# Optimization experiments

Measured on AMD Instinct MI355X. Metric: run time of the kernel, lower is better.

The kernel has to match this reference:

```python
import jax, jax.numpy as jnp
import numpy as np

B, D, L, H, P, IMG = 32, 768, 12, 12, 16, 224
N = (IMG // P) ** 2  # 196 patches
DH = D // H
FF = 4 * D
EPS = 1e-5


def _ln(x, w, b):
    m = jnp.mean(x, axis=-1, keepdims=True)
    v = jnp.mean((x - m) ** 2, axis=-1, keepdims=True)
    return (x - m) * jax.lax.rsqrt(v + EPS) * w + b


def setup_inputs() -> dict:
    key = jax.random.key(0)
    ks = jax.random.split(key, 12)
    s = 0.02
    return {
        "x": jax.random.normal(ks[0], (B, 3, IMG, IMG), jnp.float32),
        "patch_w": jax.random.normal(ks[1], (D, 3, P, P), jnp.float32) * s,
        "patch_b": jnp.zeros((D,), jnp.float32),
        "pos_embed": jax.random.normal(ks[2], (1, N, D), jnp.float32) * s,
        "ln1_w": jnp.ones((L, D), jnp.float32),
        "ln1_b": jnp.zeros((L, D), jnp.float32),
        "qkv_w": jax.random.normal(ks[3], (L, 3 * D, D), jnp.float32) * s,
        "qkv_b": jnp.zeros((L, 3 * D), jnp.float32),
        "proj_w": jax.random.normal(ks[4], (L, D, D), jnp.float32) * s,
        "proj_b": jnp.zeros((L, D), jnp.float32),
        "ln2_w": jnp.ones((L, D), jnp.float32),
        "ln2_b": jnp.zeros((L, D), jnp.float32),
        "fc1_w": jax.random.normal(ks[5], (L, FF, D), jnp.float32) * s,
        "fc1_b": jnp.zeros((L, FF), jnp.float32),
        "fc2_w": jax.random.normal(ks[6], (L, D, FF), jnp.float32) * s,
        "fc2_b": jnp.zeros((L, D), jnp.float32),
        "lnf_w": jnp.ones((D,), jnp.float32),
        "lnf_b": jnp.zeros((D,), jnp.float32),
    }


def reference(x, patch_w, patch_b, pos_embed, ln1_w, ln1_b, qkv_w, qkv_b,
              proj_w, proj_b, ln2_w, ln2_b, fc1_w, fc1_b, fc2_w, fc2_b,
              lnf_w, lnf_b):
    # Patch embed: strided conv, NCHW / OIHW
    h = jax.lax.conv_general_dilated(
        x, patch_w, window_strides=(P, P), padding="VALID",
        dimension_numbers=("NCHW", "OIHW", "NCHW")) + patch_b[None, :, None, None]
    b = h.shape[0]
    h = h.reshape(b, D, -1).transpose(0, 2, 1)  # (B, N, D)
    h = h + pos_embed  # broadcast over batch

    scale = DH ** (-0.5)
    for i in range(L):
        # --- attention (indices=None path: plain masked-free softmax) ---
        y = _ln(h, ln1_w[i], ln1_b[i])
        qkv = y @ qkv_w[i].T + qkv_b[i]                      # (B, N, 3D)
        qkv = qkv.reshape(b, -1, 3, H, DH).transpose(2, 0, 3, 1, 4)
        q, k, v = qkv[0], qkv[1], qkv[2]                     # (B, H, N, DH)
        attn = jax.nn.softmax(jnp.einsum("bhnd,bhmd->bhnm", q, k) * scale, axis=-1)
        o = jnp.einsum("bhnm,bhmd->bhnd", attn, v)
        o = o.transpose(0, 2, 1, 3).reshape(b, -1, D)
        h = h + (o @ proj_w[i].T + proj_b[i])
        # --- MLP ---
        y = _ln(h, ln2_w[i], ln2_b[i])
        y = jax.nn.gelu(y @ fc1_w[i].T + fc1_b[i], approximate=False)
        h = h + (y @ fc2_w[i].T + fc2_b[i])

    return _ln(h, lnf_w, lnf_b)
```

## Files before the change

### kernel.cpp

```cpp
#include <hip/hip_runtime.h>
#include <hip/hip_bf16.h>
#include <math.h>

#define BB    32
#define DD    768
#define LL    12
#define HH    12
#define NN    196
#define DHH   64
#define FFF   3072
#define MM    (BB * NN)
#define BHH   (BB * HH)

typedef float  floatx4 __attribute__((ext_vector_type(4)));
typedef __bf16 bf16x8  __attribute__((ext_vector_type(8)));

#define DEV __device__ __forceinline__

DEV unsigned short bf16u(float v) {
  __hip_bfloat16 h = __float2bfloat16(v);
  return __builtin_bit_cast(unsigned short, h);
}

DEV floatx4 mfma_bf16(bf16x8 a, bf16x8 b, floatx4 c) {
  return __builtin_amdgcn_mfma_f32_16x16x32_bf16(a, b, c, 0, 0, 0);
}

DEV void gl2lds16(const void* g, void* l) {
  __builtin_amdgcn_global_load_lds(
      (const __attribute__((address_space(1))) void*)g,
      (__attribute__((address_space(3))) void*)l, 16, 0, 0);
}

DEV float gelu_f(float v) {
  float ax = fabsf(v) * 0.70710678118654752f;
  float t = 1.0f / (1.0f + 0.3275911f * ax);
  float poly = t * (0.254829592f +
              t * (-0.284496736f +
              t * (1.421413741f +
              t * (-1.453152027f +
              t * 1.061405429f))));
  float er = 1.0f - poly * __expf(-ax * ax);
  er = (v < 0.0f) ? -er : er;
  return 0.5f * v * (1.0f + er);
}

DEV int xcd_swz(int orig, int nwg) {
  int q = nwg >> 3, r = nwg & 7;
  int xcd = orig & 7, pos = orig >> 3;
  int base = (xcd < r) ? xcd * (q + 1) : r * (q + 1) + (xcd - r) * q;
  return base + pos;
}

__global__ __launch_bounds__(256) void cvt4_k(const float4* __restrict__ in,
                                              ushort4* __restrict__ out, int n4) {
  int i = blockIdx.x * 256 + threadIdx.x;
  if (i < n4) {
    float4 v = in[i];
    ushort4 o;
    o.x = bf16u(v.x); o.y = bf16u(v.y); o.z = bf16u(v.z); o.w = bf16u(v.w);
    out[i] = o;
  }
}

__global__ __launch_bounds__(256) void im2col_k(const float* __restrict__ x,
                                                unsigned short* __restrict__ A) {
  int idx = blockIdx.x * 256 + threadIdx.x;
  int col = idx % DD;
  int token = idx / DD;
  int b = token / NN, p = token % NN;
  int pr = p / 14, pc = p % 14;
  int c = col >> 8, rm = col & 255, i = rm >> 4, j = rm & 15;
  float v = x[(((size_t)b * 3 + c) * 224 + pr * 16 + i) * 224 + pc * 16 + j];
  A[idx] = bf16u(v);
}

__global__ __launch_bounds__(256) void ln_k(const float* __restrict__ x,
                                            const float* __restrict__ w,
                                            const float* __restrict__ bb,
                                            unsigned short* __restrict__ outp) {
  const int token = blockIdx.x, tid = threadIdx.x;
  const float* xr = x + (size_t)token * DD;
  float v0 = xr[tid], v1 = xr[tid + 256], v2 = xr[tid + 512];
  float s = v0 + v1 + v2;
  float ss = v0 * v0 + v1 * v1 + v2 * v2;
#pragma unroll
  for (int off = 32; off; off >>= 1) {
    s += __shfl_down(s, off);
    ss += __shfl_down(ss, off);
  }
  __shared__ float rs[4], rq[4];
  if ((tid & 63) == 0) { rs[tid >> 6] = s; rq[tid >> 6] = ss; }
  __syncthreads();
  float tot = rs[0] + rs[1] + rs[2] + rs[3];
  float tq  = rq[0] + rq[1] + rq[2] + rq[3];
  const float mean = tot * (1.0f / 768.0f);
  const float var  = tq * (1.0f / 768.0f) - mean * mean;
  const float rstd = rsqrtf(var + 1e-5f);
#pragma unroll
  for (int t = 0; t < 3; t++) {
    int col = tid + t * 256;
    float xv = (t == 0) ? v0 : (t == 1 ? v1 : v2);
    float yv = (xv - mean) * rstd * w[col] + bb[col];
    outp[(size_t)token * DD + col] = bf16u(yv);
  }
}

template <int FINAL>
__global__ __launch_bounds__(256) void ln_fuse_k(float* __restrict__ h,
    const float* __restrict__ p0, const float* __restrict__ p1,
    const float* __restrict__ w, const float* __restrict__ bb,
    void* __restrict__ outp) {
  const int token = blockIdx.x, tid = threadIdx.x;
  const size_t base = (size_t)token * DD;
  float v[3];
#pragma unroll
  for (int t = 0; t < 3; t++) {
    const int col = tid + t * 256;
    v[t] = h[base + col] + p0[base + col] + p1[base + col];
    if (!FINAL) h[base + col] = v[t];
  }
  float s = v[0] + v[1] + v[2];
  float ss = v[0] * v[0] + v[1] * v[1] + v[2] * v[2];
#pragma unroll
  for (int off = 32; off; off >>= 1) {
    s += __shfl_down(s, off);
    ss += __shfl_down(ss, off);
  }
  __shared__ float rs[4], rq[4];
  if ((tid & 63) == 0) { rs[tid >> 6] = s; rq[tid >> 6] = ss; }
  __syncthreads();
  float tot = rs[0] + rs[1] + rs[2] + rs[3];
  float tq  = rq[0] + rq[1] + rq[2] + rq[3];
  const float mean = tot * (1.0f / 768.0f);
  const float var  = tq * (1.0f / 768.0f) - mean * mean;
  const float rstd = rsqrtf(var + 1e-5f);
#pragma unroll
  for (int t = 0; t < 3; t++) {
    const int col = tid + t * 256;
    float yv = (v[t] - mean) * rstd * w[col] + bb[col];
    if (FINAL) ((float*)outp)[base + col] = yv;
    else       ((unsigned short*)outp)[base + col] = bf16u(yv);
  }
}


template <int MODE>
__global__ __launch_bounds__(256, 4) void gemm_bt(
    const unsigned short* __restrict__ A, const unsigned short* __restrict__ W,
    const float* __restrict__ bias, void* __restrict__ outp, int K, int Nn) {
  __shared__ unsigned short smem[16384];
  unsigned short* As0 = smem;
  unsigned short* Bs0 = smem + 8192;
  const int tid = threadIdx.x;
  const int wave = tid >> 6, lane = tid & 63;
  const int nwg = gridDim.x * gridDim.y;
  const int wg = xcd_swz(blockIdx.x + gridDim.x * blockIdx.y, nwg);
  const int tm = (wg / gridDim.x) * 128, tn = (wg % gridDim.x) * 128;
  const int wm = (wave >> 1) * 64, wn = (wave & 1) * 64;
  const int lr = lane & 15, kq = lane >> 4;
  const int sw = (lr >> 1) & 3;
  const int koff = (kq ^ sw) * 8;
  const int c0 = tid, c1 = tid + 256;
  const int r0 = c0 >> 2, r1 = c1 >> 2;
  const int kc0 = ((c0 & 3) ^ ((r0 >> 1) & 3)) * 8;
  const int kc1 = ((c1 & 3) ^ ((r1 >> 1) & 3)) * 8;
  const size_t ga0 = (size_t)(tm + r0) * K + kc0;
  const size_t ga1 = (size_t)(tm + r1) * K + kc1;
  const size_t gb0 = (size_t)(tn + r0) * K + kc0;
  const size_t gb1 = (size_t)(tn + r1) * K + kc1;
  floatx4 acc[4][4] = {};
  auto stage = [&](int buf, int k0) {
    gl2lds16(A + ga0 + k0, As0 + buf * 4096 + c0 * 8);
    gl2lds16(A + ga1 + k0, As0 + buf * 4096 + c1 * 8);
    gl2lds16(W + gb0 + k0, Bs0 + buf * 4096 + c0 * 8);
    gl2lds16(W + gb1 + k0, Bs0 + buf * 4096 + c1 * 8);
  };
  const int nk = K >> 5;
  stage(0, 0);
  for (int it = 0; it < nk; it++) {
    const int cur = it & 1;
    __syncthreads();
    if (it + 1 < nk) stage(cur ^ 1, (it + 1) << 5);
    bf16x8 af[4], bq[4];
#pragma unroll
    for (int mi = 0; mi < 4; mi++)
      af[mi] = *(const bf16x8*)&As0[cur * 4096 + (wm + mi * 16 + lr) * 32 + koff];
#pragma unroll
    for (int ni = 0; ni < 4; ni++)
      bq[ni] = *(const bf16x8*)&Bs0[cur * 4096 + (wn + ni * 16 + lr) * 32 + koff];
#pragma unroll
    for (int mi = 0; mi < 4; mi++)
#pragma unroll
      for (int ni = 0; ni < 4; ni++)
        acc[mi][ni] = mfma_bf16(af[mi], bq[ni], acc[mi][ni]);
  }
  __syncthreads();
#pragma unroll
  for (int ni = 0; ni < 4; ni++) {
    const int lcol = wn + ni * 16 + lr;
    const float bv = bias[tn + lcol];
#pragma unroll
    for (int mi = 0; mi < 4; mi++) {
#pragma unroll
      for (int r = 0; r < 4; r++) {
        const int lrow = wm + mi * 16 + (lane >> 4) * 4 + r;
        float v = acc[mi][ni][r] + bv;
        if (MODE == 3) v = gelu_f(v);
        smem[lrow * 128 + lcol] = bf16u(v);
      }
    }
  }
  __syncthreads();
  const int tr = tid >> 4;
  const int tc = (tid & 15) * 8;
#pragma unroll
  for (int p = 0; p < 8; p++) {
    const int lrow = p * 16 + tr;
    uint4 d = *(const uint4*)&smem[lrow * 128 + tc];
    *(uint4*)&((unsigned short*)outp)[(size_t)(tm + lrow) * Nn + tn + tc] = d;
  }
}

__global__ __launch_bounds__(256, 4) void gemm_sk(
    const unsigned short* __restrict__ A, const unsigned short* __restrict__ W,
    const float* __restrict__ bias, float* __restrict__ p0,
    float* __restrict__ p1, int K, int Nn) {
  __shared__ unsigned short As[2][128 * 32];
  __shared__ unsigned short Bs[2][128 * 32];
  const int tid = threadIdx.x;
  const int wave = tid >> 6, lane = tid & 63;
  const int nwg = gridDim.x * gridDim.y;
  const int wg = xcd_swz(blockIdx.x + gridDim.x * blockIdx.y, nwg);
  const int tm = (wg / gridDim.x) * 128, tn = (wg % gridDim.x) * 128;
  const int kz = blockIdx.z;
  const int kper = K >> 1;
  const int kbase = kz * kper;
  const int wm = (wave >> 1) * 64, wn = (wave & 1) * 64;
  const int lr = lane & 15, kq = lane >> 4;
  const int sw = (lr >> 1) & 3;
  const int koff = (kq ^ sw) * 8;
  const int c0 = tid, c1 = tid + 256;
  const int r0 = c0 >> 2, r1 = c1 >> 2;
  const int kc0 = ((c0 & 3) ^ ((r0 >> 1) & 3)) * 8;
  const int kc1 = ((c1 & 3) ^ ((r1 >> 1) & 3)) * 8;
  const size_t ga0 = (size_t)(tm + r0) * K + kc0 + kbase;
  const size_t ga1 = (size_t)(tm + r1) * K + kc1 + kbase;
  const size_t gb0 = (size_t)(tn + r0) * K + kc0 + kbase;
  const size_t gb1 = (size_t)(tn + r1) * K + kc1 + kbase;
  floatx4 acc[4][4] = {};
  auto stage = [&](int buf, int k0) {
    gl2lds16(A + ga0 + k0, &As[buf][c0 * 8]);
    gl2lds16(A + ga1 + k0, &As[buf][c1 * 8]);
    gl2lds16(W + gb0 + k0, &Bs[buf][c0 * 8]);
    gl2lds16(W + gb1 + k0, &Bs[buf][c1 * 8]);
  };
  const int nk = kper >> 5;
  stage(0, 0);
  for (int it = 0; it < nk; it++) {
    const int cur = it & 1;
    __syncthreads();
    if (it + 1 < nk) stage(cur ^ 1, (it + 1) << 5);
    bf16x8 af[4], bq[4];
#pragma unroll
    for (int mi = 0; mi < 4; mi++)
      af[mi] = *(const bf16x8*)&As[cur][(wm + mi * 16 + lr) * 32 + koff];
#pragma unroll
    for (int ni = 0; ni < 4; ni++)
      bq[ni] = *(const bf16x8*)&Bs[cur][(wn + ni * 16 + lr) * 32 + koff];
#pragma unroll
    for (int mi = 0; mi < 4; mi++)
#pragma unroll
      for (int ni = 0; ni < 4; ni++)
        acc[mi][ni] = mfma_bf16(af[mi], bq[ni], acc[mi][ni]);
  }
  float* __restrict__ po = kz ? p1 : p0;
  const int rbase = tm + wm + (lane >> 4) * 4;
  const int cbase = tn + wn + lr;
#pragma unroll
  for (int ni = 0; ni < 4; ni++) {
    const int col = cbase + ni * 16;
    const float bv = kz ? 0.0f : bias[col];
#pragma unroll
    for (int mi = 0; mi < 4; mi++) {
#pragma unroll
      for (int r = 0; r < 4; r++) {
        const int row = rbase + mi * 16 + r;
        po[(size_t)row * Nn + col] = acc[mi][ni][r] + bv;
      }
    }
  }
}

template <int MODE>
__global__ __launch_bounds__(256, 4) void gemm64_bt(
    const unsigned short* __restrict__ A, const unsigned short* __restrict__ W,
    const float* __restrict__ bias, const float* __restrict__ aux,
    float* __restrict__ outp, int K, int Nn) {
  __shared__ unsigned short As[2][64 * 32];
  __shared__ unsigned short Bs[2][128 * 32];
  const int tid = threadIdx.x;
  const int wave = tid >> 6, lane = tid & 63;
  const int tm = blockIdx.y * 64, tn = blockIdx.x * 128;
  const int wm = (wave >> 1) * 32, wn = (wave & 1) * 64;
  const int lr = lane & 15, kq = lane >> 4;
  const int sw = (lr >> 1) & 3;
  const int koff = (kq ^ sw) * 8;
  const int ra = tid >> 2;
  const int kca = ((tid & 3) ^ ((ra >> 1) & 3)) * 8;
  const int c0 = tid, c1 = tid + 256;
  const int r0 = c0 >> 2, r1 = c1 >> 2;
  const int kc0 = ((c0 & 3) ^ ((r0 >> 1) & 3)) * 8;
  const int kc1 = ((c1 & 3) ^ ((r1 >> 1) & 3)) * 8;
  const size_t ga  = (size_t)(tm + ra) * K + kca;
  const size_t gb0 = (size_t)(tn + r0) * K + kc0;
  const size_t gb1 = (size_t)(tn + r1) * K + kc1;
  floatx4 acc[2][4] = {};
  auto stage = [&](int buf, int k0) {
    gl2lds16(A + ga + k0, &As[buf][tid * 8]);
    gl2lds16(W + gb0 + k0, &Bs[buf][c0 * 8]);
    gl2lds16(W + gb1 + k0, &Bs[buf][c1 * 8]);
  };
  const int nk = K >> 5;
  stage(0, 0);
  for (int it = 0; it < nk; it++) {
    const int cur = it & 1;
    __syncthreads();
    if (it + 1 < nk) stage(cur ^ 1, (it + 1) << 5);
    bf16x8 af[2], bq[4];
#pragma unroll
    for (int mi = 0; mi < 2; mi++)
      af[mi] = *(const bf16x8*)&As[cur][(wm + mi * 16 + lr) * 32 + koff];
#pragma unroll
    for (int ni = 0; ni < 4; ni++)
      bq[ni] = *(const bf16x8*)&Bs[cur][(wn + ni * 16 + lr) * 32 + koff];
#pragma unroll
    for (int mi = 0; mi < 2; mi++)
#pragma unroll
      for (int ni = 0; ni < 4; ni++)
        acc[mi][ni] = mfma_bf16(af[mi], bq[ni], acc[mi][ni]);
  }
  const int rbase = tm + wm + (lane >> 4) * 4;
  const int cbase = tn + wn + lr;
#pragma unroll
  for (int ni = 0; ni < 4; ni++) {
    const int col = cbase + ni * 16;
    const float bv = bias[col];
#pragma unroll
    for (int mi = 0; mi < 2; mi++) {
#pragma unroll
      for (int r = 0; r < 4; r++) {
        const int row = rbase + mi * 16 + r;
        float v = acc[mi][ni][r] + bv;
        float* hp = outp + (size_t)row * Nn + col;
        if (MODE == 1) *hp = v + aux[(size_t)(row % NN) * Nn + col];
        else           *hp = *hp + v;
      }
    }
  }
}

__global__ __launch_bounds__(256) void attn_sm_k(const unsigned short* __restrict__ qkv,
                                                 unsigned short* __restrict__ P) {
  __shared__ float S[32][232];
  const int tid = threadIdx.x;
  const int bh = blockIdx.x;
  const int b = bh / HH, hh = bh % HH;
  const int i0 = blockIdx.y * 32;
  const int wave = tid >> 6, lane = tid & 63;
  const int lr = lane & 15, k8 = (lane >> 4) * 8;
  for (int t = wave; t < 28; t += 4) {
    const int til = (t / 14) * 16, tj = (t % 14) * 16;
    const int iq = min(i0 + til + lr, NN - 1), jk = min(tj + lr, NN - 1);
    const unsigned short* qb = qkv + (size_t)(b * NN + iq) * 2304 + hh * 64 + k8;
    const unsigned short* kb = qkv + (size_t)(b * NN + jk) * 2304 + 768 + hh * 64 + k8;
    floatx4 acc = {0.f, 0.f, 0.f, 0.f};
    acc = mfma_bf16(*(const bf16x8*)qb, *(const bf16x8*)kb, acc);
    acc = mfma_bf16(*(const bf16x8*)(qb + 32), *(const bf16x8*)(kb + 32), acc);
#pragma unroll
    for (int r = 0; r < 4; r++)
      S[til + (lane >> 4) * 4 + r][tj + lr] = acc[r] * 0.125f;
  }
  __syncthreads();
  const int row = tid >> 3, sub = tid & 7;
  float v[28];
  float m = -1e30f;
#pragma unroll
  for (int t = 0; t < 28; t++) {
    const int c = sub + t * 8;
    v[t] = (c < NN) ? S[row][c] : -1e30f;
    m = fmaxf(m, v[t]);
  }
  m = fmaxf(m, __shfl_xor(m, 1));
  m = fmaxf(m, __shfl_xor(m, 2));
  m = fmaxf(m, __shfl_xor(m, 4));
  float s = 0.f;
#pragma unroll
  for (int t = 0; t < 28; t++) {
    v[t] = (sub + t * 8 < NN) ? __expf(v[t] - m) : 0.f;
    s += v[t];
  }
  s += __shfl_xor(s, 1);
  s += __shfl_xor(s, 2);
  s += __shfl_xor(s, 4);
  const float inv = 1.0f / s;
  const int gi = i0 + row;
  if (gi < NN) {
    unsigned short* prow = P + ((size_t)bh * NN + gi) * 224;
#pragma unroll
    for (int t = 0; t < 28; t++) prow[sub + t * 8] = bf16u(v[t] * inv);
  }
}

__global__ __launch_bounds__(256) void vt_k(const unsigned short* __restrict__ qkv,
                                            unsigned short* __restrict__ Vt) {
  int idx = blockIdx.x * 256 + threadIdx.x;
  int j = idx % 224;
  int rest = idx / 224;
  int d = rest % 64, bh = rest / 64;
  int b = bh / HH, hh = bh % HH;
  unsigned short val = 0;
  if (j < NN) val = qkv[(size_t)(b * NN + j) * 2304 + 1536 + hh * 64 + d];
  Vt[idx] = val;
}

__global__ __launch_bounds__(256) void pv_k(const unsigned short* __restrict__ P,
                                            const unsigned short* __restrict__ Vt,
                                            unsigned short* __restrict__ o) {
  const int bh = blockIdx.x;
  const int b = bh / HH, hh = bh % HH;
  const int t = blockIdx.y * 4 + (threadIdx.x >> 6);
  const int it = t >> 2, dt = t & 3;
  const int lane = threadIdx.x & 63, lr = lane & 15, k8 = (lane >> 4) * 8;
  const int ip = min(it * 16 + lr, NN - 1);
  const unsigned short* pb = P + ((size_t)bh * NN + ip) * 224 + k8;
  const unsigned short* vb = Vt + ((size_t)bh * 64 + dt * 16 + lr) * 224 + k8;
  floatx4 acc = {0.f, 0.f, 0.f, 0.f};
#pragma unroll
  for (int k0 = 0; k0 < 224; k0 += 32)
    acc = mfma_bf16(*(const bf16x8*)(pb + k0), *(const bf16x8*)(vb + k0), acc);
#pragma unroll
  for (int r = 0; r < 4; r++) {
    int i = it * 16 + (lane >> 4) * 4 + r;
    if (i < NN)
      o[(size_t)(b * NN + i) * DD + hh * 64 + dt * 16 + lr] = bf16u(acc[r]);
  }
}

extern "C" void kernel_launch(void* const* d_in, const int* in_sizes, int n_in,
                              void* d_out, int out_size, void* d_ws, size_t ws_size,
                              hipStream_t stream) {
  const float* x       = (const float*)d_in[0];
  const float* patchw  = (const float*)d_in[1];
  const float* patchb  = (const float*)d_in[2];
  const float* pos     = (const float*)d_in[3];
  const float* ln1w    = (const float*)d_in[4];
  const float* ln1b    = (const float*)d_in[5];
  const float* qkvw    = (const float*)d_in[6];
  const float* qkvb    = (const float*)d_in[7];
  const float* projw   = (const float*)d_in[8];
  const float* projb   = (const float*)d_in[9];
  const float* ln2w    = (const float*)d_in[10];
  const float* ln2b    = (const float*)d_in[11];
  const float* fc1w    = (const float*)d_in[12];
  const float* fc1b    = (const float*)d_in[13];
  const float* fc2w    = (const float*)d_in[14];
  const float* fc2b    = (const float*)d_in[15];
  const float* lnfw    = (const float*)d_in[16];
  const float* lnfb    = (const float*)d_in[17];

  char* base = (char*)d_ws;
  size_t off = 0;
  auto alloc = [&](size_t bytes) {
    void* p = base + off;
    off = (off + bytes + 255) & ~(size_t)255;
    return p;
  };
  unsigned short* Wq  = (unsigned short*)alloc((size_t)LL * 2304 * 768 * 2);
  unsigned short* Wp  = (unsigned short*)alloc((size_t)LL * 768 * 768 * 2);
  unsigned short* W1  = (unsigned short*)alloc((size_t)LL * 3072 * 768 * 2);
  unsigned short* W2  = (unsigned short*)alloc((size_t)LL * 768 * 3072 * 2);
  unsigned short* Wpe = (unsigned short*)alloc((size_t)768 * 768 * 2);
  float*          h   = (float*)alloc((size_t)MM * DD * 4);
  unsigned short* y   = (unsigned short*)alloc((size_t)MM * DD * 2);
  unsigned short* qkv = (unsigned short*)alloc((size_t)MM * 2304 * 2);
  unsigned short* g   = (unsigned short*)alloc((size_t)MM * FFF * 2);
  unsigned short* P   = (unsigned short*)alloc((size_t)BHH * NN * 224 * 2);
  unsigned short* Vt  = (unsigned short*)alloc((size_t)BHH * 64 * 224 * 2);
  unsigned short* o   = (unsigned short*)alloc((size_t)MM * DD * 2);
  if (off > ws_size) return;

  unsigned short* Aim = qkv;
  float* pp0 = (float*)qkv;
  float* pp1 = (float*)P;

  auto cvt = [&](const float* src, unsigned short* dst, size_t n) {
    int n4 = (int)(n / 4);
    cvt4_k<<<dim3((n4 + 255) / 256), dim3(256), 0, stream>>>(
        (const float4*)src, (ushort4*)dst, n4);
  };
  cvt(qkvw, Wq, (size_t)LL * 2304 * 768);
  cvt(projw, Wp, (size_t)LL * 768 * 768);
  cvt(fc1w, W1, (size_t)LL * 3072 * 768);
  cvt(fc2w, W2, (size_t)LL * 768 * 3072);
  cvt(patchw, Wpe, (size_t)768 * 768);

  im2col_k<<<dim3(MM * DD / 256), dim3(256), 0, stream>>>(x, Aim);
  gemm64_bt<1><<<dim3(6, 98), dim3(256), 0, stream>>>(Aim, Wpe, patchb, pos, h, 768, 768);

  ln_k<<<dim3(MM), dim3(256), 0, stream>>>(h, ln1w, ln1b, y);

  for (int l = 0; l < LL; l++) {
    gemm_bt<0><<<dim3(18, 49), dim3(256), 0, stream>>>(
        y, Wq + (size_t)l * 2304 * 768, qkvb + l * 2304, qkv, 768, 2304);
    attn_sm_k<<<dim3(BHH, 7), dim3(256), 0, stream>>>(qkv, P);
    vt_k<<<dim3(BHH * 64 * 224 / 256), dim3(256), 0, stream>>>(qkv, Vt);
    pv_k<<<dim3(BHH, 13), dim3(256), 0, stream>>>(P, Vt, o);
    gemm_sk<<<dim3(6, 49, 2), dim3(256), 0, stream>>>(
        o, Wp + (size_t)l * 768 * 768, projb + l * 768, pp0, pp1, 768, 768);
    ln_fuse_k<0><<<dim3(MM), dim3(256), 0, stream>>>(
        h, pp0, pp1, ln2w + l * 768, ln2b + l * 768, y);
    gemm_bt<3><<<dim3(24, 49), dim3(256), 0, stream>>>(
        y, W1 + (size_t)l * 3072 * 768, fc1b + l * 3072, g, 768, 3072);
    gemm_sk<<<dim3(6, 49, 2), dim3(256), 0, stream>>>(
        g, W2 + (size_t)l * 768 * 3072, fc2b + l * 768, pp0, pp1, 3072, 768);
    if (l + 1 < LL) {
      ln_fuse_k<0><<<dim3(MM), dim3(256), 0, stream>>>(
          h, pp0, pp1, ln1w + (l + 1) * 768, ln1b + (l + 1) * 768, y);
    } else {
      ln_fuse_k<1><<<dim3(MM), dim3(256), 0, stream>>>(
          h, pp0, pp1, lnfw, lnfb, d_out);
    }
  }
}
```

Measured before the change: 3.506 ms.

## Fuse softmax and PV matmul into one attention kernel via LDS

The softmax kernel now keeps the normalized probabilities in a shared-memory bf16 tile and immediately multiplies them by the transposed V, so the separate PV kernel and the global P buffer disappear. This removes a round trip of the roughly 30 MB probability matrix through global memory and one launch per layer. The price is extra LDS per block (about 15 KB more), which may lower occupancy. The former P buffer is reallocated as a dedicated fp32 partial-sum buffer.

```diff
diff --git a/kernel.cpp b/kernel.cpp
--- a/kernel.cpp
+++ b/kernel.cpp
@@ -360,9 +360,11 @@
   }
 }
 
-__global__ __launch_bounds__(256) void attn_sm_k(const unsigned short* __restrict__ qkv,
-                                                 unsigned short* __restrict__ P) {
+__global__ __launch_bounds__(256) void attn_fused_k(
+    const unsigned short* __restrict__ qkv, const unsigned short* __restrict__ Vt,
+    unsigned short* __restrict__ o) {
   __shared__ float S[32][232];
+  __shared__ __align__(16) unsigned short Pl[32][232];
   const int tid = threadIdx.x;
   const int bh = blockIdx.x;
   const int b = bh / HH, hh = bh % HH;
@@ -404,11 +406,25 @@
   s += __shfl_xor(s, 2);
   s += __shfl_xor(s, 4);
   const float inv = 1.0f / s;
-  const int gi = i0 + row;
-  if (gi < NN) {
-    unsigned short* prow = P + ((size_t)bh * NN + gi) * 224;
-#pragma unroll
-    for (int t = 0; t < 28; t++) prow[sub + t * 8] = bf16u(v[t] * inv);
+#pragma unroll
+  for (int t = 0; t < 28; t++) Pl[row][sub + t * 8] = bf16u(v[t] * inv);
+  __syncthreads();
+#pragma unroll
+  for (int w = 0; w < 2; w++) {
+    const int tt = wave * 2 + w;
+    const int it = tt >> 2, dt = tt & 3;
+    const unsigned short* vb = Vt + ((size_t)bh * 64 + dt * 16 + lr) * 224 + k8;
+    floatx4 acc = {0.f, 0.f, 0.f, 0.f};
+#pragma unroll
+    for (int k0 = 0; k0 < 224; k0 += 32)
+      acc = mfma_bf16(*(const bf16x8*)&Pl[it * 16 + lr][k8 + k0],
+                      *(const bf16x8*)(vb + k0), acc);
+#pragma unroll
+    for (int r = 0; r < 4; r++) {
+      const int i = i0 + it * 16 + (lane >> 4) * 4 + r;
+      if (i < NN)
+        o[(size_t)(b * NN + i) * DD + hh * 64 + dt * 16 + lr] = bf16u(acc[r]);
+    }
   }
 }
 
@@ -422,29 +438,6 @@
   unsigned short val = 0;
   if (j < NN) val = qkv[(size_t)(b * NN + j) * 2304 + 1536 + hh * 64 + d];
   Vt[idx] = val;
-}
-
-__global__ __launch_bounds__(256) void pv_k(const unsigned short* __restrict__ P,
-                                            const unsigned short* __restrict__ Vt,
-                                            unsigned short* __restrict__ o) {
-  const int bh = blockIdx.x;
-  const int b = bh / HH, hh = bh % HH;
-  const int t = blockIdx.y * 4 + (threadIdx.x >> 6);
-  const int it = t >> 2, dt = t & 3;
-  const int lane = threadIdx.x & 63, lr = lane & 15, k8 = (lane >> 4) * 8;
-  const int ip = min(it * 16 + lr, NN - 1);
-  const unsigned short* pb = P + ((size_t)bh * NN + ip) * 224 + k8;
-  const unsigned short* vb = Vt + ((size_t)bh * 64 + dt * 16 + lr) * 224 + k8;
-  floatx4 acc = {0.f, 0.f, 0.f, 0.f};
-#pragma unroll
-  for (int k0 = 0; k0 < 224; k0 += 32)
-    acc = mfma_bf16(*(const bf16x8*)(pb + k0), *(const bf16x8*)(vb + k0), acc);
-#pragma unroll
-  for (int r = 0; r < 4; r++) {
-    int i = it * 16 + (lane >> 4) * 4 + r;
-    if (i < NN)
-      o[(size_t)(b * NN + i) * DD + hh * 64 + dt * 16 + lr] = bf16u(acc[r]);
-  }
 }
 
 extern "C" void kernel_launch(void* const* d_in, const int* in_sizes, int n_in,
@@ -485,14 +478,13 @@
   unsigned short* y   = (unsigned short*)alloc((size_t)MM * DD * 2);
   unsigned short* qkv = (unsigned short*)alloc((size_t)MM * 2304 * 2);
   unsigned short* g   = (unsigned short*)alloc((size_t)MM * FFF * 2);
-  unsigned short* P   = (unsigned short*)alloc((size_t)BHH * NN * 224 * 2);
+  float*          pp1 = (float*)alloc((size_t)MM * DD * 4);
   unsigned short* Vt  = (unsigned short*)alloc((size_t)BHH * 64 * 224 * 2);
   unsigned short* o   = (unsigned short*)alloc((size_t)MM * DD * 2);
   if (off > ws_size) return;
 
   unsigned short* Aim = qkv;
   float* pp0 = (float*)qkv;
-  float* pp1 = (float*)P;
 
   auto cvt = [&](const float* src, unsigned short* dst, size_t n) {
     int n4 = (int)(n / 4);
@@ -513,9 +505,8 @@
   for (int l = 0; l < LL; l++) {
     gemm_bt<0><<<dim3(18, 49), dim3(256), 0, stream>>>(
         y, Wq + (size_t)l * 2304 * 768, qkvb + l * 2304, qkv, 768, 2304);
-    attn_sm_k<<<dim3(BHH, 7), dim3(256), 0, stream>>>(qkv, P);
     vt_k<<<dim3(BHH * 64 * 224 / 256), dim3(256), 0, stream>>>(qkv, Vt);
-    pv_k<<<dim3(BHH, 13), dim3(256), 0, stream>>>(P, Vt, o);
+    attn_fused_k<<<dim3(BHH, 7), dim3(256), 0, stream>>>(qkv, Vt, o);
     gemm_sk<<<dim3(6, 49, 2), dim3(256), 0, stream>>>(
         o, Wp + (size_t)l * 768 * 768, projb + l * 768, pp0, pp1, 768, 768);
     ln_fuse_k<0><<<dim3(MM), dim3(256), 0, stream>>>(
```

Result: faster. 3.347 ms (-4.5%).
